# Kernel tuning notes

Hardware: AMD Instinct MI355X
Metric: run time of the kernel (lower is better)

The kernel has to match this reference:

```python
import jax, jax.numpy as jnp
import numpy as np

D_MODEL = 512
NUM_HEADS = 8
DEPTH = D_MODEL // NUM_HEADS
EPS = 1e-08


def _phi(x):
    # feature map: elu(x) + 1 (strictly positive, as in 'Transformers are RNNs')
    return jax.nn.elu(x) + 1.0


def setup_inputs() -> dict:
    key = jax.random.key(0)
    ks = jax.random.split(key, 9)
    B, S = 4, 8192
    scale = 1.0 / np.sqrt(D_MODEL)
    return {
        "q": jax.random.normal(ks[0], (B, S, D_MODEL), jnp.float32),
        "k": jax.random.normal(ks[1], (B, S, D_MODEL), jnp.float32),
        "v": jax.random.normal(ks[2], (B, S, D_MODEL), jnp.float32),
        "wq": jax.random.normal(ks[3], (D_MODEL, D_MODEL), jnp.float32) * scale,
        "bq": jnp.zeros((D_MODEL,), jnp.float32),
        "wk": jax.random.normal(ks[4], (D_MODEL, D_MODEL), jnp.float32) * scale,
        "bk": jnp.zeros((D_MODEL,), jnp.float32),
        "wv": jax.random.normal(ks[5], (D_MODEL, D_MODEL), jnp.float32) * scale,
        "bv": jnp.zeros((D_MODEL,), jnp.float32),
    }


def reference(q, k, v, wq, bq, wk, bk, wv, bv):
    B, S, _ = q.shape
    # projections
    qp = q @ wq + bq
    kp = k @ wk + bk
    vp = v @ wv + bv
    # split heads -> [B, S, H, D]
    qh = _phi(qp.reshape(B, S, NUM_HEADS, DEPTH))
    kh = _phi(kp.reshape(B, S, NUM_HEADS, DEPTH))
    vh = vp.reshape(B, S, NUM_HEADS, DEPTH)
    # kv state: [B, D, E, H]
    kv = jnp.einsum('bshd,bshe->bdeh', kh, vh)
    # normalizer
    k_red = jnp.sum(kh, axis=1) + EPS                    # [B, H, D]
    z = 1.0 / jnp.einsum('blhd,bhd->blh', qh, k_red)     # [B, L, H]
    out = jnp.einsum('blhd,bdeh,blh->blhe', qh, kv, z)   # [B, L, H, E]
    return out.reshape(B, S, NUM_HEADS * DEPTH)
```

## Files before the change

kernel.cpp:

```cpp
#include <hip/hip_runtime.h>
#include <hip/hip_bf16.h>

#define DM 512
#define HEADS 8
#define DEPTH 64
#define BATCH 4
#define SEQ 8192
#define MROWS (BATCH*SEQ)

using short8 = __attribute__((ext_vector_type(8))) short;
using floatx4 = __attribute__((ext_vector_type(4))) float;

#define AS1 __attribute__((address_space(1)))
#define AS3 __attribute__((address_space(3)))

static __device__ __forceinline__ float bf2f(unsigned short u) {
    union { unsigned int i; float f; } x; x.i = ((unsigned int)u) << 16; return x.f;
}
static __device__ __forceinline__ unsigned short f2bf(float f) {
    union { float f; unsigned int i; } x; x.f = f;
    unsigned int i = x.i;
    return (unsigned short)((i + 0x7FFFu + ((i >> 16) & 1u)) >> 16);
}
static __device__ __forceinline__ unsigned int pack2_rtz(float a, float b) {
    union { float f; unsigned int u; } x, y; x.f = a; y.f = b;
    return (x.u >> 16) | (y.u & 0xFFFF0000u);
}
static __device__ __forceinline__ void gl_lds16(const unsigned short* g, unsigned short* l) {
    __builtin_amdgcn_global_load_lds((const AS1 unsigned int*)g, (AS3 unsigned int*)l, 16, 0, 0);
}

__global__ __launch_bounds__(256) void wprep_kernel(const float* __restrict__ wq,
                                                    const float* __restrict__ wk,
                                                    const float* __restrict__ wv,
                                                    unsigned short* __restrict__ wqT,
                                                    unsigned short* __restrict__ wkT,
                                                    unsigned short* __restrict__ wvT) {
    const float* w = blockIdx.y == 0 ? wq : (blockIdx.y == 1 ? wk : wv);
    unsigned short* wT = blockIdx.y == 0 ? wqT : (blockIdx.y == 1 ? wkT : wvT);
    int idx = blockIdx.x * 256 + threadIdx.x;
    int k = idx & (DM - 1);
    int n = idx >> 9;
    wT[n * DM + k] = f2bf(w[k * DM + n]);
}

__global__ __launch_bounds__(512) void proj3_kernel(
        const float* __restrict__ q, const float* __restrict__ k, const float* __restrict__ v,
        const unsigned short* __restrict__ wqT, const unsigned short* __restrict__ wkT,
        const unsigned short* __restrict__ wvT,
        const float* __restrict__ bq, const float* __restrict__ bk, const float* __restrict__ bv,
        unsigned short* __restrict__ qh, unsigned short* __restrict__ kh,
        unsigned short* __restrict__ vh) {
    __shared__ unsigned short As[128][72];
    __shared__ unsigned short Bs[256 * 64];

    const int t = threadIdx.x;
    const int w = t >> 6;
    const int l15 = t & 15;
    const int g = (t >> 4) & 3;

    const int which = blockIdx.y;
    const float* X = which == 0 ? q : (which == 1 ? k : v);
    const unsigned short* WT = which == 0 ? wqT : (which == 1 ? wkT : wvT);
    const float* bias = which == 0 ? bq : (which == 1 ? bk : bv);
    unsigned short* Y = which == 0 ? qh : (which == 1 ? kh : vh);
    const bool phi = (which < 2);

    const int flat = blockIdx.x;
    const int wg = (flat & 7) * 64 + (flat >> 3);
    const int m0 = (wg >> 1) * 128;
    const int n0 = (wg & 1) * 256;
    const int wr = (w >> 2) * 64;
    const int wc = (w & 3) * 64;

    const int arow = t >> 2;
    const int aq16 = (t & 3) * 16;
    const float* xp = X + (size_t)(m0 + arow) * DM + aq16;

    const unsigned short* gbl[4];
    unsigned short* lbw[4];
    #pragma unroll
    for (int i = 0; i < 4; ++i) {
        int c = i * 512 + t;
        int r = c >> 3, p = c & 7;
        gbl[i] = WT + (size_t)(n0 + r) * DM + p * 8;
        lbw[i] = Bs + r * 64 + (p ^ (r & 7)) * 8;
    }

    float bvx[4];
    #pragma unroll
    for (int n = 0; n < 4; ++n) bvx[n] = bias[n0 + wc + n * 16 + l15];

    floatx4 acc[4][4] = {};
    float4 av0, av1, av2, av3;
    int4 br0, br1, br2, br3;

    av0 = *(const float4*)xp;        av1 = *(const float4*)(xp + 4);
    av2 = *(const float4*)(xp + 8);  av3 = *(const float4*)(xp + 12);
    br0 = *(const int4*)gbl[0];      br1 = *(const int4*)gbl[1];
    br2 = *(const int4*)gbl[2];      br3 = *(const int4*)gbl[3];

    #pragma unroll 1
    for (int tile = 0; tile < 8; ++tile) {
        __syncthreads();
        *(int4*)lbw[0] = br0; *(int4*)lbw[1] = br1;
        *(int4*)lbw[2] = br2; *(int4*)lbw[3] = br3;
        *(uint4*)&As[arow][aq16] = make_uint4(pack2_rtz(av0.x, av0.y), pack2_rtz(av0.z, av0.w),
                                              pack2_rtz(av1.x, av1.y), pack2_rtz(av1.z, av1.w));
        *(uint4*)&As[arow][aq16 + 8] = make_uint4(pack2_rtz(av2.x, av2.y), pack2_rtz(av2.z, av2.w),
                                                  pack2_rtz(av3.x, av3.y), pack2_rtz(av3.z, av3.w));
        if (tile < 7) {
            const int koff = tile * 64 + 64;
            av0 = *(const float4*)(xp + koff);      av1 = *(const float4*)(xp + koff + 4);
            av2 = *(const float4*)(xp + koff + 8);  av3 = *(const float4*)(xp + koff + 12);
            br0 = *(const int4*)(gbl[0] + koff);    br1 = *(const int4*)(gbl[1] + koff);
            br2 = *(const int4*)(gbl[2] + koff);    br3 = *(const int4*)(gbl[3] + koff);
        }
        __syncthreads();
        #pragma unroll
        for (int kk = 0; kk < 2; ++kk) {
            short8 af[4], bfr[4];
            #pragma unroll
            for (int m = 0; m < 4; ++m)
                af[m] = *(const short8*)&As[wr + m * 16 + l15][kk * 32 + g * 8];
            #pragma unroll
            for (int n = 0; n < 4; ++n) {
                int r = wc + n * 16 + l15;
                int ch = (kk * 4 + g) ^ (r & 7);
                bfr[n] = *(const short8*)&Bs[r * 64 + ch * 8];
            }
            #pragma unroll
            for (int m = 0; m < 4; ++m)
                #pragma unroll
                for (int n = 0; n < 4; ++n)
                    acc[m][n] = __builtin_amdgcn_mfma_f32_16x16x32_bf16(af[m], bfr[n], acc[m][n], 0, 0, 0);
        }
    }

    #pragma unroll
    for (int n = 0; n < 4; ++n) {
        int col = n0 + wc + n * 16 + l15;
        float bb = bvx[n];
        #pragma unroll
        for (int m = 0; m < 4; ++m) {
            #pragma unroll
            for (int j = 0; j < 4; ++j) {
                int row = m0 + wr + m * 16 + g * 4 + j;
                float val = acc[m][n][j] + bb;
                if (phi) val = (val > 0.0f) ? (val + 1.0f) : __expf(val);
                Y[(size_t)row * DM + col] = f2bf(val);
            }
        }
    }
}

#define KV_CHUNK 256
#define KV_TILE 32
__global__ __launch_bounds__(256) void kv_kernel(const unsigned short* __restrict__ kh,
                                                 const unsigned short* __restrict__ vh,
                                                 float* __restrict__ kv,
                                                 float* __restrict__ kred) {
    __shared__ unsigned short khT[64][40];
    __shared__ unsigned short vhT[64][40];

    const int t = threadIdx.x;
    const int w = t >> 6;
    const int l15 = t & 15;
    const int g = (t >> 4) & 3;
    const int b = blockIdx.z, h = blockIdx.y;
    const int s0 = blockIdx.x * KV_CHUNK;

    const int s_i = t >> 3;
    const int d0 = (t & 7) * 8;

    const size_t gbase = ((size_t)b * SEQ + s0 + s_i) * DM + h * DEPTH + d0;

    short8 ones;
    #pragma unroll
    for (int i = 0; i < 8; ++i) ones[i] = (short)0x3F80;

    floatx4 acc[5] = {};

    int4 kr = *(const int4*)(kh + gbase);
    int4 vr = *(const int4*)(vh + gbase);

    #pragma unroll
    for (int tile = 0; tile < KV_CHUNK / KV_TILE; ++tile) {
        {
            const unsigned short* kk = (const unsigned short*)&kr;
            const unsigned short* vv = (const unsigned short*)&vr;
            #pragma unroll
            for (int i = 0; i < 8; ++i) khT[d0 + i][s_i] = kk[i];
            #pragma unroll
            for (int i = 0; i < 8; ++i) vhT[d0 + i][s_i] = vv[i];
        }
        if (tile + 1 < KV_CHUNK / KV_TILE) {
            size_t off = gbase + (size_t)(tile + 1) * KV_TILE * DM;
            kr = *(const int4*)(kh + off);
            vr = *(const int4*)(vh + off);
        }
        __syncthreads();

        short8 af = *(const short8*)&khT[w * 16 + l15][g * 8];
        short8 bf0 = *(const short8*)&vhT[0 * 16 + l15][g * 8];
        short8 bf1 = *(const short8*)&vhT[1 * 16 + l15][g * 8];
        short8 bf2 = *(const short8*)&vhT[2 * 16 + l15][g * 8];
        short8 bf3 = *(const short8*)&vhT[3 * 16 + l15][g * 8];
        acc[0] = __builtin_amdgcn_mfma_f32_16x16x32_bf16(af, bf0, acc[0], 0, 0, 0);
        acc[1] = __builtin_amdgcn_mfma_f32_16x16x32_bf16(af, bf1, acc[1], 0, 0, 0);
        acc[2] = __builtin_amdgcn_mfma_f32_16x16x32_bf16(af, bf2, acc[2], 0, 0, 0);
        acc[3] = __builtin_amdgcn_mfma_f32_16x16x32_bf16(af, ones, acc[3], 0, 0, 0);
        acc[4] = __builtin_amdgcn_mfma_f32_16x16x32_bf16(af, bf3, acc[4], 0, 0, 0);
        __syncthreads();
    }

    float* kvp = kv + (size_t)(b * HEADS + h) * (DEPTH * DEPTH);
    #pragma unroll
    for (int j = 0; j < 4; ++j) {
        int drow = w * 16 + g * 4 + j;
        atomicAdd(&kvp[drow * DEPTH + 0 * 16 + l15], acc[0][j]);
        atomicAdd(&kvp[drow * DEPTH + 1 * 16 + l15], acc[1][j]);
        atomicAdd(&kvp[drow * DEPTH + 2 * 16 + l15], acc[2][j]);
        atomicAdd(&kvp[drow * DEPTH + 3 * 16 + l15], acc[4][j]);
    }
    if (l15 == 0) {
        float* krp = kred + (b * HEADS + h) * DEPTH;
        #pragma unroll
        for (int j = 0; j < 4; ++j)
            atomicAdd(&krp[w * 16 + g * 4 + j], acc[3][j]);
    }
}

__global__ __launch_bounds__(256) void out_kernel(const unsigned short* __restrict__ qh,
                                                  const float* __restrict__ kv,
                                                  const float* __restrict__ kred,
                                                  float* __restrict__ out) {
    __shared__ unsigned short Qs[256 * 64];
    __shared__ unsigned short KVTs[80][72];

    const int t = threadIdx.x;
    const int l = t & 63;
    const int w = t >> 6;
    const int l15 = l & 15;
    const int g = l >> 4;
    const int b = blockIdx.z, h = blockIdx.y;
    const int s0 = blockIdx.x * 256;
    const int wr = w * 64;

    const size_t qbase = ((size_t)b * SEQ + s0) * DM + h * DEPTH;
    #pragma unroll
    for (int i = 0; i < 8; ++i) {
        int c = i * 256 + t;
        int r = c >> 3;
        int gp = c & 7;
        int gd = gp ^ (r & 7);
        const unsigned short* gsrc = qh + qbase + (size_t)r * DM + gd * 8;
        unsigned short* ldst = Qs + ((size_t)i * 256 + w * 64) * 8;
        gl_lds16(gsrc, ldst);
    }

    const float* kvp = kv + (size_t)(b * HEADS + h) * (DEPTH * DEPTH);
    const float* krp = kred + (size_t)(b * HEADS + h) * DEPTH;
    #pragma unroll
    for (int j = 0; j < 20; ++j) {
        int f = j * 256 + t;
        int e = f >> 6, d = f & 63;
        float val = (e < 64) ? kvp[d * DEPTH + e]
                  : (e == 64 ? (krp[d] + 1e-8f) : 0.0f);
        KVTs[e][d] = f2bf(val);
    }

    __syncthreads();

    short8 af[2][4], bfr[2][5];
    #pragma unroll
    for (int kk = 0; kk < 2; ++kk) {
        #pragma unroll
        for (int m = 0; m < 4; ++m) {
            int r = wr + m * 16 + l15;
            int ch = (kk * 4 + g) ^ (r & 7);
            af[kk][m] = *(const short8*)(Qs + r * 64 + ch * 8);
        }
        #pragma unroll
        for (int n = 0; n < 5; ++n)
            bfr[kk][n] = *(const short8*)&KVTs[n * 16 + l15][kk * 32 + g * 8];
    }

    floatx4 acc[4][5] = {};
    #pragma unroll
    for (int kk = 0; kk < 2; ++kk)
        #pragma unroll
        for (int m = 0; m < 4; ++m)
            #pragma unroll
            for (int n = 0; n < 5; ++n)
                acc[m][n] = __builtin_amdgcn_mfma_f32_16x16x32_bf16(af[kk][m], bfr[kk][n], acc[m][n], 0, 0, 0);

    float* op = out + ((size_t)b * SEQ + s0) * DM + h * DEPTH;
    #pragma unroll
    for (int m = 0; m < 4; ++m) {
        #pragma unroll
        for (int j = 0; j < 4; ++j) {
            float den = __shfl(acc[m][4][j], l & 48);
            float z = 1.0f / den;
            int row = wr + m * 16 + g * 4 + j;
            #pragma unroll
            for (int n = 0; n < 4; ++n)
                op[(size_t)row * DM + n * 16 + l15] = acc[m][n][j] * z;
        }
    }
}

extern "C" void kernel_launch(void* const* d_in, const int* in_sizes, int n_in,
                              void* d_out, int out_size, void* d_ws, size_t ws_size,
                              hipStream_t stream) {
    const float* q  = (const float*)d_in[0];
    const float* k  = (const float*)d_in[1];
    const float* v  = (const float*)d_in[2];
    const float* wq = (const float*)d_in[3];
    const float* bq = (const float*)d_in[4];
    const float* wk = (const float*)d_in[5];
    const float* bk = (const float*)d_in[6];
    const float* wv = (const float*)d_in[7];
    const float* bv = (const float*)d_in[8];
    float* out = (float*)d_out;

    char* ws = (char*)d_ws;
    const size_t sz_h = (size_t)MROWS * DM * 2;
    unsigned short* qh  = (unsigned short*)(ws);
    unsigned short* kh  = (unsigned short*)(ws + sz_h);
    unsigned short* vh  = (unsigned short*)(ws + 2 * sz_h);
    unsigned short* wqT = (unsigned short*)(ws + 3 * sz_h);
    unsigned short* wkT = wqT + DM * DM;
    unsigned short* wvT = wkT + DM * DM;
    float* kvbuf   = (float*)(ws + 3 * sz_h + (size_t)3 * DM * DM * 2);
    float* kredbuf = kvbuf + BATCH * HEADS * DEPTH * DEPTH;

    hipMemsetAsync(kvbuf, 0,
                   (size_t)(BATCH * HEADS * DEPTH * DEPTH + BATCH * HEADS * DEPTH) * sizeof(float),
                   stream);

    wprep_kernel<<<dim3(DM * DM / 256, 3), 256, 0, stream>>>(wq, wk, wv, wqT, wkT, wvT);

    proj3_kernel<<<dim3(512, 3), 512, 0, stream>>>(q, k, v, wqT, wkT, wvT,
                                                   bq, bk, bv, qh, kh, vh);

    kv_kernel<<<dim3(SEQ / KV_CHUNK, HEADS, BATCH), 256, 0, stream>>>(kh, vh, kvbuf, kredbuf);
    out_kernel<<<dim3(SEQ / 256, HEADS, BATCH), 256, 0, stream>>>(qh, kvbuf, kredbuf, out);
}
```

Baseline: 190.3 us.

## Load projection weight fragments directly from global, shrink proj tile to 64 rows

After: 225.8 us. 1.19x slower.

```diff
diff --git a/kernel.cpp b/kernel.cpp
--- a/kernel.cpp
+++ b/kernel.cpp
@@ -44,15 +44,14 @@
     wT[n * DM + k] = f2bf(w[k * DM + n]);
 }
 
-__global__ __launch_bounds__(512) void proj3_kernel(
+__global__ __launch_bounds__(256) void proj3_kernel(
         const float* __restrict__ q, const float* __restrict__ k, const float* __restrict__ v,
         const unsigned short* __restrict__ wqT, const unsigned short* __restrict__ wkT,
         const unsigned short* __restrict__ wvT,
         const float* __restrict__ bq, const float* __restrict__ bk, const float* __restrict__ bv,
         unsigned short* __restrict__ qh, unsigned short* __restrict__ kh,
         unsigned short* __restrict__ vh) {
-    __shared__ unsigned short As[128][72];
-    __shared__ unsigned short Bs[256 * 64];
+    __shared__ unsigned short As[64][72];
 
     const int t = threadIdx.x;
     const int w = t >> 6;
@@ -67,25 +66,19 @@
     const bool phi = (which < 2);
 
     const int flat = blockIdx.x;
-    const int wg = (flat & 7) * 64 + (flat >> 3);
-    const int m0 = (wg >> 1) * 128;
+    const int wg = (flat & 7) * 128 + (flat >> 3);
+    const int m0 = (wg >> 1) * 64;
     const int n0 = (wg & 1) * 256;
-    const int wr = (w >> 2) * 64;
-    const int wc = (w & 3) * 64;
+    const int wc = w * 64;
 
     const int arow = t >> 2;
     const int aq16 = (t & 3) * 16;
     const float* xp = X + (size_t)(m0 + arow) * DM + aq16;
 
-    const unsigned short* gbl[4];
-    unsigned short* lbw[4];
-    #pragma unroll
-    for (int i = 0; i < 4; ++i) {
-        int c = i * 512 + t;
-        int r = c >> 3, p = c & 7;
-        gbl[i] = WT + (size_t)(n0 + r) * DM + p * 8;
-        lbw[i] = Bs + r * 64 + (p ^ (r & 7)) * 8;
-    }
+    const unsigned short* wrow[4];
+    #pragma unroll
+    for (int n = 0; n < 4; ++n)
+        wrow[n] = WT + (size_t)(n0 + wc + n * 16 + l15) * DM;
 
     float bvx[4];
     #pragma unroll
@@ -93,18 +86,13 @@
 
     floatx4 acc[4][4] = {};
     float4 av0, av1, av2, av3;
-    int4 br0, br1, br2, br3;
 
     av0 = *(const float4*)xp;        av1 = *(const float4*)(xp + 4);
     av2 = *(const float4*)(xp + 8);  av3 = *(const float4*)(xp + 12);
-    br0 = *(const int4*)gbl[0];      br1 = *(const int4*)gbl[1];
-    br2 = *(const int4*)gbl[2];      br3 = *(const int4*)gbl[3];
 
     #pragma unroll 1
     for (int tile = 0; tile < 8; ++tile) {
         __syncthreads();
-        *(int4*)lbw[0] = br0; *(int4*)lbw[1] = br1;
-        *(int4*)lbw[2] = br2; *(int4*)lbw[3] = br3;
         *(uint4*)&As[arow][aq16] = make_uint4(pack2_rtz(av0.x, av0.y), pack2_rtz(av0.z, av0.w),
                                               pack2_rtz(av1.x, av1.y), pack2_rtz(av1.z, av1.w));
         *(uint4*)&As[arow][aq16 + 8] = make_uint4(pack2_rtz(av2.x, av2.y), pack2_rtz(av2.z, av2.w),
@@ -113,22 +101,18 @@
             const int koff = tile * 64 + 64;
             av0 = *(const float4*)(xp + koff);      av1 = *(const float4*)(xp + koff + 4);
             av2 = *(const float4*)(xp + koff + 8);  av3 = *(const float4*)(xp + koff + 12);
-            br0 = *(const int4*)(gbl[0] + koff);    br1 = *(const int4*)(gbl[1] + koff);
-            br2 = *(const int4*)(gbl[2] + koff);    br3 = *(const int4*)(gbl[3] + koff);
         }
         __syncthreads();
+        const int koff = tile * 64;
         #pragma unroll
         for (int kk = 0; kk < 2; ++kk) {
             short8 af[4], bfr[4];
             #pragma unroll
+            for (int n = 0; n < 4; ++n)
+                bfr[n] = *(const short8*)(wrow[n] + koff + kk * 32 + g * 8);
+            #pragma unroll
             for (int m = 0; m < 4; ++m)
-                af[m] = *(const short8*)&As[wr + m * 16 + l15][kk * 32 + g * 8];
-            #pragma unroll
-            for (int n = 0; n < 4; ++n) {
-                int r = wc + n * 16 + l15;
-                int ch = (kk * 4 + g) ^ (r & 7);
-                bfr[n] = *(const short8*)&Bs[r * 64 + ch * 8];
-            }
+                af[m] = *(const short8*)&As[m * 16 + l15][kk * 32 + g * 8];
             #pragma unroll
             for (int m = 0; m < 4; ++m)
                 #pragma unroll
@@ -145,7 +129,7 @@
         for (int m = 0; m < 4; ++m) {
             #pragma unroll
             for (int j = 0; j < 4; ++j) {
-                int row = m0 + wr + m * 16 + g * 4 + j;
+                int row = m0 + m * 16 + g * 4 + j;
                 float val = acc[m][n][j] + bb;
                 if (phi) val = (val > 0.0f) ? (val + 1.0f) : __expf(val);
                 Y[(size_t)row * DM + col] = f2bf(val);
@@ -341,8 +325,8 @@
 
     wprep_kernel<<<dim3(DM * DM / 256, 3), 256, 0, stream>>>(wq, wk, wv, wqT, wkT, wvT);
 
-    proj3_kernel<<<dim3(512, 3), 512, 0, stream>>>(q, k, v, wqT, wkT, wvT,
-                                                   bq, bk, bv, qh, kh, vh);
+    proj3_kernel<<<dim3(1024, 3), 256, 0, stream>>>(q, k, v, wqT, wkT, wvT,
+                                                    bq, bk, bv, qh, kh, vh);
 
     kv_kernel<<<dim3(SEQ / KV_CHUNK, HEADS, BATCH), 256, 0, stream>>>(kh, vh, kvbuf, kredbuf);
     out_kernel<<<dim3(SEQ / 256, HEADS, BATCH), 256, 0, stream>>>(qh, kvbuf, kredbuf, out);
```
